# Kernel tuning notes

Measured on AMD Instinct MI355X. Metric: run time of the kernel, lower is better.

The kernel has to match this reference:

```python
import jax, jax.numpy as jnp
import numpy as np

THRESHOLD = 0.1
N_HEAD = 16
NEG_INF = -1e9


def setup_inputs() -> dict:
    key = jax.random.key(0)
    ks = jax.random.split(key, 8)
    B, T, C = 2, 2048, 1024
    H, D, R = N_HEAD, C // N_HEAD, 8
    return {
        "x": jax.random.normal(ks[0], (B, T, C), dtype=jnp.float32),
        "W_attn": jax.random.normal(ks[1], (C, 3 * C), dtype=jnp.float32) * 0.02,
        "W_proj": jax.random.normal(ks[2], (C, C), dtype=jnp.float32) * 0.02,
        "W_recip": jax.random.normal(ks[3], (D, R), dtype=jnp.float32) * 0.02,
        "w_std": jax.random.uniform(ks[4], (H,), dtype=jnp.float32),
        "w_rec": jax.random.uniform(ks[5], (H,), dtype=jnp.float32),
        "w_disc": jax.random.uniform(ks[6], (H,), dtype=jnp.float32),
        "d_bias": jax.random.normal(ks[7], (H, T), dtype=jnp.float32) * 0.02,
    }


def reference(x, W_attn, W_proj, W_recip, w_std, w_rec, w_disc, d_bias):
    B, T, C = x.shape
    H = N_HEAD
    D = C // H
    R = W_recip.shape[1]
    D_std = D - R

    # QKV projection (Linear without bias)
    qkv = x @ W_attn  # [B,T,3C]
    q, k, v = jnp.split(qkv, 3, axis=2)

    def to_heads(t):
        return t.reshape(B, T, H, D).transpose(0, 2, 1, 3)  # [B,H,T,D]

    q, k, v = to_heads(q), to_heads(k), to_heads(v)

    # low-rank reciprocal projections
    QW = q @ W_recip  # [B,H,T,R]
    KW = k @ W_recip

    ws = jnp.sqrt(jnp.clip(w_std, 1e-8))[:, None, None]  # [H,1,1]
    wr = jnp.sqrt(jnp.clip(w_rec, 1e-8))[:, None, None]
    use_ra = (w_rec > THRESHOLD)[:, None, None]  # [H,1,1]

    # RA heads: augmented Q/K = [ws*Q_std | wr*KW] / [ws*K_std | wr*QW]
    q_aug = jnp.concatenate([ws * q[..., :D_std], wr * KW], axis=-1)
    k_aug = jnp.concatenate([ws * k[..., :D_std], wr * QW], axis=-1)
    q_eff = jnp.where(use_ra, q_aug, ws * q)
    k_eff = jnp.where(use_ra, k_aug, ws * k)

    # mean-centered discoverability column bias: [1,H,1,T]
    d = d_bias[:, :T]
    d = d - d.mean(axis=-1, keepdims=True)
    bias = (d * w_disc[:, None])[None, :, None, :]

    scale = 1.0 / jnp.sqrt(jnp.asarray(D, dtype=x.dtype))
    scores = jnp.einsum("bhid,bhjd->bhij", q_eff, k_eff) * scale + bias
    causal = jnp.tril(jnp.ones((T, T), dtype=bool))
    scores = jnp.where(causal[None, None], scores, NEG_INF)
    attn = jax.nn.softmax(scores, axis=-1)
    out = jnp.einsum("bhij,bhjd->bhid", attn, v)  # [B,H,T,D]

    out = out.transpose(0, 2, 1, 3).reshape(B, T, C)
    return out @ W_proj
```

## Files before the change

### kernel.cpp

```cpp
#include <hip/hip_runtime.h>
#include <hip/hip_bf16.h>

#define DEVI __device__ __forceinline__

typedef __attribute__((ext_vector_type(8))) short short8;
typedef __attribute__((ext_vector_type(4))) short short4v;
typedef __attribute__((ext_vector_type(4))) float floatx4;

static constexpr int B_ = 2, T_ = 2048, C_ = 1024, H_ = 16, D_ = 64;
static constexpr float LOG2E = 1.44269504088896f;

DEVI float bf2f(unsigned short u) {
    union { unsigned int i; float f; } v; v.i = ((unsigned int)u) << 16; return v.f;
}
DEVI unsigned short f2bf(float f) {
    union { float f; unsigned int i; } v; v.f = f;
    unsigned int x = v.i;
    return (unsigned short)((x + 0x7fffu + ((x >> 16) & 1u)) >> 16);
}
DEVI unsigned int pk2bf(float lo, float hi) {
#if __has_builtin(__builtin_amdgcn_cvt_pk_bf16_f32)
    typedef __attribute__((ext_vector_type(2))) __bf16 bf16x2;
    union { bf16x2 v; unsigned int u; } r;
    r.v = __builtin_amdgcn_cvt_pk_bf16_f32(lo, hi);
    return r.u;
#else
    return (unsigned int)f2bf(lo) | ((unsigned int)f2bf(hi) << 16);
#endif
}
DEVI float fast_exp2(float x) {
#if __has_builtin(__builtin_amdgcn_exp2f)
    return __builtin_amdgcn_exp2f(x);
#else
    return __expf(x * 0.6931471805599453f);
#endif
}

DEVI void async16(const unsigned short* g, unsigned short* l) {
    __builtin_amdgcn_global_load_lds((const __attribute__((address_space(1))) void*)g,
                                     (__attribute__((address_space(3))) void*)l, 16, 0, 0);
}

DEVI void tr_body(const float* in, unsigned short* out, int K, int N, int bx, int by,
                  int tid, float (*tile)[65], float scale, bool skiphi) {
    int k0 = by * 64, n0 = bx * 64;
#pragma unroll
    for (int r = 0; r < 4; r++) {
        int ci = tid + r * 256;
        int row = ci >> 4, c4 = (ci & 15) * 4;
        float4 v = *(const float4*)&in[(size_t)(k0 + row) * N + n0 + c4];
        tile[row][c4 + 0] = v.x; tile[row][c4 + 1] = v.y;
        tile[row][c4 + 2] = v.z; tile[row][c4 + 3] = v.w;
    }
    __syncthreads();
#pragma unroll
    for (int r = 0; r < 2; r++) {
        int ci = tid + r * 256;
        int row = ci >> 3, c8 = (ci & 7) * 8;
        if (skiphi && row >= 56) continue;
        union { unsigned short u[8]; short8 s; } o;
#pragma unroll
        for (int j = 0; j < 8; j++) o.u[j] = f2bf(tile[c8 + j][row] * scale);
        *(short8*)&out[(size_t)(n0 + row) * K + k0 + c8] = o.s;
    }
}

__global__ __launch_bounds__(256) void k_prep(const float* __restrict__ x,
                                              const float* __restrict__ W_attn,
                                              const float* __restrict__ W_proj,
                                              const float* __restrict__ d_bias,
                                              const float* __restrict__ w_disc,
                                              const float* __restrict__ W_recip,
                                              const float* __restrict__ w_std,
                                              const float* __restrict__ w_rec,
                                              unsigned short* __restrict__ x_bf,
                                              unsigned short* __restrict__ wa_t,
                                              unsigned short* __restrict__ wp_t,
                                              float* __restrict__ bias) {
    __shared__ float tile[64][65];
    __shared__ float red[256];
    int bid = blockIdx.x, tid = threadIdx.x;
    if (bid < 2048) {
        int i = bid * 256 + tid;
        const float4* p = (const float4*)x + (size_t)i * 2;
        float4 a = p[0], b = p[1];
        union { unsigned short u[8]; short8 s; } r;
        r.u[0] = f2bf(a.x); r.u[1] = f2bf(a.y); r.u[2] = f2bf(a.z); r.u[3] = f2bf(a.w);
        r.u[4] = f2bf(b.x); r.u[5] = f2bf(b.y); r.u[6] = f2bf(b.z); r.u[7] = f2bf(b.w);
        *(short8*)&x_bf[(size_t)i * 8] = r.s;
    } else if (bid < 2816) {
        int idx = bid - 2048;
        int bx = idx % 48, by = idx / 48;
        int sec = bx >> 4, h = bx & 15;
        float ws = sqrtf(fmaxf(w_std[h], 1e-8f));
        float sc = (sec == 0) ? ws * (0.125f * LOG2E) : (sec == 1 ? ws : 1.0f);
        tr_body(W_attn, wa_t, 1024, 3072, bx, by, tid, tile, sc, sec < 2);
    } else if (bid < 3072) {
        int idx = bid - 2816;
        tr_body(W_proj, wp_t, 1024, 1024, idx & 15, idx >> 4, tid, tile, 1.0f, false);
    } else if (bid < 3088) {
        int h = bid - 3072;
        float s = 0.f;
        for (int t = tid; t < T_; t += 256) s += d_bias[h * T_ + t];
        red[tid] = s;
        __syncthreads();
        for (int st = 128; st > 0; st >>= 1) {
            if (tid < st) red[tid] += red[tid + st];
            __syncthreads();
        }
        float mean = red[0] * (1.0f / T_);
        float wd = w_disc[h] * LOG2E;
        for (int t = tid; t < T_; t += 256) bias[h * T_ + t] = (d_bias[h * T_ + t] - mean) * wd;
    } else {
        int idx = bid - 3088;
        int h = idx & 15, side = idx >> 4;
        float* WrS = &tile[0][0];
        for (int i = tid; i < 512; i += 256) WrS[i] = W_recip[i];
        __syncthreads();
        float wrv = sqrtf(fmaxf(w_rec[h], 1e-8f));
        float wsv = sqrtf(fmaxf(w_std[h], 1e-8f));
        bool ra = w_rec[h] > 0.1f;
        float sc = (side == 0 ? 0.125f * LOG2E : 1.0f) * (ra ? wrv : wsv);
        int dst0 = side * 1024 + h * 64 + 56;
        for (int kk = tid; kk < 1024; kk += 256) {
            const float* srow = W_attn + (size_t)kk * 3072;
            float out[8];
            if (ra) {
                int sc0 = (1 - side) * 1024 + h * 64;
#pragma unroll
                for (int r = 0; r < 8; r++) out[r] = 0.f;
                for (int dd = 0; dd < 64; dd++) {
                    float v = srow[sc0 + dd];
#pragma unroll
                    for (int r = 0; r < 8; r++) out[r] += v * WrS[dd * 8 + r];
                }
            } else {
                int sc0 = side * 1024 + h * 64 + 56;
#pragma unroll
                for (int r = 0; r < 8; r++) out[r] = srow[sc0 + r];
            }
#pragma unroll
            for (int r = 0; r < 8; r++)
                wa_t[(size_t)(dst0 + r) * 1024 + kk] = f2bf(sc * out[r]);
        }
    }
}

__global__ __launch_bounds__(256) void k_gemm_qkv(const unsigned short* __restrict__ A,
                                                  const unsigned short* __restrict__ Bt,
                                                  unsigned short* __restrict__ qe,
                                                  unsigned short* __restrict__ ke,
                                                  unsigned short* __restrict__ vt,
                                                  int M, int N, int K) {
    union SM {
        unsigned short buf[4][128 * 32];
        unsigned short stg[4][4096];
    };
    __shared__ __align__(16) SM sm;
    int b1d = blockIdx.y * 24 + blockIdx.x;
    int xcd = b1d & 7, i6 = b1d >> 3;
    int bx = (xcd & 1) * 12 + i6 % 12;
    int by = (xcd >> 1) * 8 + i6 / 12;
    int m0 = by * 128, n0 = bx * 128;
    int tid = threadIdx.x, l = tid & 63, w = tid >> 6;
    int wm = (w >> 1) * 64, wn = (w & 1) * 64;
    int lm = l & 15, lq = l >> 4;
    floatx4 acc[4][4];
#pragma unroll
    for (int a = 0; a < 4; a++)
#pragma unroll
        for (int b = 0; b < 4; b++) acc[a][b] = {0.f, 0.f, 0.f, 0.f};

    for (int k0 = 0; k0 < K; k0 += 64) {
        __syncthreads();
#pragma unroll
        for (int r = 0; r < 2; r++) {
            int ci = tid + r * 256;
            int row = ci >> 2, off = (ci & 3) * 8;
            async16(&A[(size_t)(m0 + row) * K + k0 + off],       &sm.buf[0][row * 32 + off]);
            async16(&A[(size_t)(m0 + row) * K + k0 + 32 + off],  &sm.buf[1][row * 32 + off]);
            async16(&Bt[(size_t)(n0 + row) * K + k0 + off],      &sm.buf[2][row * 32 + off]);
            async16(&Bt[(size_t)(n0 + row) * K + k0 + 32 + off], &sm.buf[3][row * 32 + off]);
        }
        __syncthreads();
#pragma unroll
        for (int half = 0; half < 2; half++) {
            const unsigned short* Ah = sm.buf[half];
            const unsigned short* Bh = sm.buf[2 + half];
            short8 af[4], bf[4];
#pragma unroll
            for (int t = 0; t < 4; t++) af[t] = *(short8*)&Ah[(wm + t * 16 + lm) * 32 + lq * 8];
#pragma unroll
            for (int t = 0; t < 4; t++) bf[t] = *(short8*)&Bh[(wn + t * 16 + lm) * 32 + lq * 8];
#pragma unroll
            for (int tm = 0; tm < 4; tm++)
#pragma unroll
                for (int tn = 0; tn < 4; tn++)
                    acc[tm][tn] = __builtin_amdgcn_mfma_f32_16x16x32_bf16(af[tm], bf[tn], acc[tm][tn], 0, 0, 0);
        }
    }
    __syncthreads();
    int sec = bx >> 3;
    int b = by >> 4;
    int head = ((n0 & 1023) >> 6) + (wn >> 6);
    size_t bhbase = (size_t)(b * 16 + head) * 131072;
    int tloc0 = (m0 & 2047) + wm;
    unsigned short* dst = (sec == 0) ? qe : (sec == 1) ? ke : vt;
    unsigned short* S = sm.stg[w];
    if (sec < 2) {
#pragma unroll
        for (int tm = 0; tm < 4; tm++)
#pragma unroll
            for (int tn = 0; tn < 4; tn++) {
                int base = tm * 1024 + (tn >> 1) * 512 + ((tn & 1) * 2 + (lm >> 3)) * 128 +
                           (lm & 7) + lq * 32;
#pragma unroll
                for (int r = 0; r < 4; r++) S[base + r * 8] = f2bf(acc[tm][tn][r]);
            }
    } else {
#pragma unroll
        for (int tm = 0; tm < 4; tm++)
#pragma unroll
            for (int tn = 0; tn < 4; tn++) {
                int base = (tm >> 1) * 2048 + tn * 512 + ((tm & 1) * 2 + (lq >> 1)) * 128 +
                           lm * 8 + (lq & 1) * 4;
                union { unsigned short u[4]; short4v s4; } o;
#pragma unroll
                for (int r = 0; r < 4; r++) o.u[r] = f2bf(acc[tm][tn][r]);
                *(short4v*)&S[base] = o.s4;
            }
    }
    size_t gbase = bhbase + ((sec < 2) ? (size_t)(tloc0 >> 4) * 1024
                                       : (size_t)(tloc0 >> 5) * 2048);
#pragma unroll
    for (int i = 0; i < 8; i++) {
        short8 v = *(const short8*)&S[(size_t)(i * 64 + l) * 8];
        *(short8*)&dst[gbase + (size_t)(i * 64 + l) * 8] = v;
    }
}

__global__ __launch_bounds__(256) void k_gemm64(const unsigned short* __restrict__ A,
                                                const unsigned short* __restrict__ Bt,
                                                float* __restrict__ C, int M, int N, int K) {
    __shared__ __align__(16) unsigned short As[2][128 * 32];
    __shared__ __align__(16) unsigned short Bs[2][64 * 32];
    int b1d = blockIdx.y * 16 + blockIdx.x;
    int xcd = b1d & 7, i6 = b1d >> 3;
    int bx = (xcd & 1) * 8 + (i6 & 7);
    int by = (xcd >> 1) * 8 + (i6 >> 3);
    int m0 = by * 128, n0 = bx * 64;
    int tid = threadIdx.x, l = tid & 63, w = tid >> 6;
    int wm = w * 32;
    int lm = l & 15, lq = l >> 4;
    floatx4 acc[2][4];
#pragma unroll
    for (int a = 0; a < 2; a++)
#pragma unroll
        for (int b = 0; b < 4; b++) acc[a][b] = {0.f, 0.f, 0.f, 0.f};

    for (int k0 = 0; k0 < K; k0 += 64) {
        __syncthreads();
#pragma unroll
        for (int r = 0; r < 2; r++) {
            int ci = tid + r * 256;
            int row = ci >> 2, off = (ci & 3) * 8;
            async16(&A[(size_t)(m0 + row) * K + k0 + off],      &As[0][row * 32 + off]);
            async16(&A[(size_t)(m0 + row) * K + k0 + 32 + off], &As[1][row * 32 + off]);
        }
        {
            int row = tid >> 2, off = (tid & 3) * 8;
            async16(&Bt[(size_t)(n0 + row) * K + k0 + off],      &Bs[0][row * 32 + off]);
            async16(&Bt[(size_t)(n0 + row) * K + k0 + 32 + off], &Bs[1][row * 32 + off]);
        }
        __syncthreads();
#pragma unroll
        for (int half = 0; half < 2; half++) {
            short8 af[2], bf[4];
#pragma unroll
            for (int t = 0; t < 2; t++) af[t] = *(short8*)&As[half][(wm + t * 16 + lm) * 32 + lq * 8];
#pragma unroll
            for (int t = 0; t < 4; t++) bf[t] = *(short8*)&Bs[half][(t * 16 + lm) * 32 + lq * 8];
#pragma unroll
            for (int tm = 0; tm < 2; tm++)
#pragma unroll
                for (int tn = 0; tn < 4; tn++)
                    acc[tm][tn] = __builtin_amdgcn_mfma_f32_16x16x32_bf16(af[tm], bf[tn], acc[tm][tn], 0, 0, 0);
        }
    }
#pragma unroll
    for (int tm = 0; tm < 2; tm++)
#pragma unroll
        for (int tn = 0; tn < 4; tn++) {
            int row = m0 + wm + tm * 16 + lq * 4;
            int col = n0 + tn * 16 + lm;
#pragma unroll
            for (int r = 0; r < 4; r++) C[(size_t)(row + r) * N + col] = acc[tm][tn][r];
        }
}

DEVI void exp_pack(float sv[4][4], float& l_part, unsigned int pk[4][2]) {
#pragma unroll
    for (int js = 0; js < 4; js++)
#pragma unroll
        for (int r = 0; r < 4; r++) {
            float p = fast_exp2(sv[js][r]);
            sv[js][r] = p;
            l_part += p;
        }
#pragma unroll
    for (int js = 0; js < 4; js++) {
        pk[js][0] = pk2bf(sv[js][0], sv[js][1]);
        pk[js][1] = pk2bf(sv[js][2], sv[js][3]);
    }
}

DEVI short8 make_pf(const unsigned int pk[4][2], int c, int srcLo, int srcHi, bool hi) {
    int a0 = __shfl((int)pk[2 * c][0], srcLo);
    int a1 = __shfl((int)pk[2 * c][1], srcLo);
    int a2 = __shfl((int)pk[2 * c][0], srcHi);
    int a3 = __shfl((int)pk[2 * c][1], srcHi);
    int b0 = __shfl((int)pk[2 * c + 1][0], srcLo);
    int b1 = __shfl((int)pk[2 * c + 1][1], srcLo);
    int b2 = __shfl((int)pk[2 * c + 1][0], srcHi);
    int b3 = __shfl((int)pk[2 * c + 1][1], srcHi);
    union { int i[4]; short8 s; } pf;
    pf.i[0] = hi ? b0 : a0;
    pf.i[1] = hi ? b1 : a1;
    pf.i[2] = hi ? b2 : a2;
    pf.i[3] = hi ? b3 : a3;
    return pf.s;
}

struct KF { short8 lo[4]; short8 hi[4]; };

__global__ __launch_bounds__(256) void k_attn(const unsigned short* __restrict__ qe,
                                              const unsigned short* __restrict__ ke,
                                              const unsigned short* __restrict__ vt,
                                              const float* __restrict__ bias,
                                              unsigned short* __restrict__ obf) {
    __shared__ __align__(16) float psum[2][64][36];
    int b1d = blockIdx.y * 32 + blockIdx.x;
    int xcd = b1d & 7, j = b1d >> 3;
    int bh = xcd * 4 + (j >> 5);
    int pxq = j & 31;
    int b = bh >> 4, h = bh & 15;
    int tid = threadIdx.x, l = tid & 63, w = tid >> 6;
    int pairL = w >> 1;
    int phase = w & 1;
    int lm = l & 15, lq = l >> 4;
    int l8 = l * 8;
    const size_t hb = (size_t)bh * 131072;
    const unsigned short* qeh = qe + hb;
    const unsigned short* keh = ke + hb;
    const unsigned short* vth = vt + hb;
    const float* biash = bias + h * T_;

    int gA = pxq * 2 + pairL;
    int gB = 127 - gA;
    int itA = (gA >> 2) + 1, itB = (gB >> 2) + 1;
    int irowA = gA * 16 + lm, irowB = gB * 16 + lm;

    short8 qA0 = *(const short8*)(qeh + (size_t)gA * 1024 + l8);
    short8 qA1 = *(const short8*)(qeh + (size_t)gA * 1024 + 512 + l8);
    short8 qB0 = *(const short8*)(qeh + (size_t)gB * 1024 + l8);
    short8 qB1 = *(const short8*)(qeh + (size_t)gB * 1024 + 512 + l8);

    floatx4 OA[4], OB[4];
#pragma unroll
    for (int i = 0; i < 4; i++) { OA[i] = {0.f, 0.f, 0.f, 0.f}; OB[i] = {0.f, 0.f, 0.f, 0.f}; }
    float lA = 0.f, lB = 0.f;

    const int srcLo = ((lq & 1) * 2) * 16 + lm;
    const int srcHi = srcLo + 16;
    const bool hi = (lq >> 1) & 1;

    KF kfa, kfb;
#pragma unroll
    for (int js = 0; js < 4; js++) {
        const unsigned short* kp = keh + (size_t)phase * 4096 + (size_t)js * 1024 + l8;
        kfa.lo[js] = *(const short8*)kp;
        kfa.hi[js] = *(const short8*)(kp + 512);
    }

    auto step = [&](int s, KF& cur, KF& nxt) {
        int j0 = s * 64;
        bool doA = (s < itA);
        bool maskA = (s == itA - 1);
        bool maskB = (s == itB - 1);
        {
            const unsigned short* kb = keh + (size_t)(s + 2) * 4096 + l8;
#pragma unroll
            for (int js = 0; js < 4; js++) {
                nxt.lo[js] = *(const short8*)(kb + js * 1024);
                nxt.hi[js] = *(const short8*)(kb + js * 1024 + 512);
            }
        }
        short8 vfr[2][4];
#pragma unroll
        for (int c = 0; c < 2; c++)
#pragma unroll
            for (int dt = 0; dt < 4; dt++)
                vfr[c][dt] = *(const short8*)(vth + (size_t)((j0 >> 5) + c) * 2048 + dt * 512 + l8);
        float bv[4][4];
#pragma unroll
        for (int js = 0; js < 4; js++) {
            float4 bj = *(const float4*)&biash[j0 + js * 16 + lq * 4];
            bv[js][0] = bj.x; bv[js][1] = bj.y; bv[js][2] = bj.z; bv[js][3] = bj.w;
        }
        floatx4 sb4[4], sa4[4];
#pragma unroll
        for (int js = 0; js < 4; js++) {
            floatx4 sb = {0.f, 0.f, 0.f, 0.f};
            sb = __builtin_amdgcn_mfma_f32_16x16x32_bf16(cur.lo[js], qB0, sb, 0, 0, 0);
            sb = __builtin_amdgcn_mfma_f32_16x16x32_bf16(cur.hi[js], qB1, sb, 0, 0, 0);
            sb4[js] = sb;
        }
        if (doA) {
#pragma unroll
            for (int js = 0; js < 4; js++) {
                floatx4 sa = {0.f, 0.f, 0.f, 0.f};
                sa = __builtin_amdgcn_mfma_f32_16x16x32_bf16(cur.lo[js], qA0, sa, 0, 0, 0);
                sa = __builtin_amdgcn_mfma_f32_16x16x32_bf16(cur.hi[js], qA1, sa, 0, 0, 0);
                sa4[js] = sa;
            }
        }
        float svB[4][4];
#pragma unroll
        for (int js = 0; js < 4; js++)
#pragma unroll
            for (int r = 0; r < 4; r++) svB[js][r] = sb4[js][r] + bv[js][r];
        if (maskB) {
#pragma unroll
            for (int js = 0; js < 4; js++) {
                int jb = j0 + js * 16 + lq * 4;
#pragma unroll
                for (int r = 0; r < 4; r++)
                    if (jb + r > irowB) svB[js][r] = -1e9f;
            }
        }
        unsigned int pkB[4][2];
        exp_pack(svB, lB, pkB);

        if (doA) {
            float svA[4][4];
#pragma unroll
            for (int js = 0; js < 4; js++)
#pragma unroll
                for (int r = 0; r < 4; r++) svA[js][r] = sa4[js][r] + bv[js][r];
            if (maskA) {
#pragma unroll
                for (int js = 0; js < 4; js++) {
                    int jb = j0 + js * 16 + lq * 4;
#pragma unroll
                    for (int r = 0; r < 4; r++)
                        if (jb + r > irowA) svA[js][r] = -1e9f;
                }
            }
            unsigned int pkA[4][2];
            exp_pack(svA, lA, pkA);
#pragma unroll
            for (int c = 0; c < 2; c++) {
                short8 pfA = make_pf(pkA, c, srcLo, srcHi, hi);
                short8 pfB = make_pf(pkB, c, srcLo, srcHi, hi);
#pragma unroll
                for (int dt = 0; dt < 4; dt++) {
                    OA[dt] = __builtin_amdgcn_mfma_f32_16x16x32_bf16(vfr[c][dt], pfA, OA[dt], 0, 0, 0);
                    OB[dt] = __builtin_amdgcn_mfma_f32_16x16x32_bf16(vfr[c][dt], pfB, OB[dt], 0, 0, 0);
                }
            }
        } else {
#pragma unroll
            for (int c = 0; c < 2; c++) {
                short8 pfB = make_pf(pkB, c, srcLo, srcHi, hi);
#pragma unroll
                for (int dt = 0; dt < 4; dt++)
                    OB[dt] = __builtin_amdgcn_mfma_f32_16x16x32_bf16(vfr[c][dt], pfB, OB[dt], 0, 0, 0);
            }
        }
    };

    int s = phase;
    for (; s + 2 < itB; s += 4) {
        step(s, kfa, kfb);
        step(s + 2, kfb, kfa);
    }
    if (s < itB) step(s, kfa, kfb);

    if (phase == 1) {
        float* dst = psum[pairL][l];
#pragma unroll
        for (int dt = 0; dt < 4; dt++) *(floatx4*)&dst[dt * 4] = OA[dt];
#pragma unroll
        for (int dt = 0; dt < 4; dt++) *(floatx4*)&dst[16 + dt * 4] = OB[dt];
        dst[32] = lA; dst[33] = lB;
    }
    __syncthreads();
    if (phase == 1) return;
    {
        const float* src = psum[pairL][l];
#pragma unroll
        for (int dt = 0; dt < 4; dt++) {
            OA[dt] += *(const floatx4*)&src[dt * 4];
            OB[dt] += *(const floatx4*)&src[16 + dt * 4];
        }
        lA += src[32]; lB += src[33];
    }

    lA += __shfl_xor(lA, 16); lA += __shfl_xor(lA, 32);
    lB += __shfl_xor(lB, 16); lB += __shfl_xor(lB, 32);
    {
        float inv = 1.0f / lA;
        unsigned short* orow = obf + (size_t)(b * T_ + irowA) * C_ + h * 64;
#pragma unroll
        for (int dt = 0; dt < 4; dt++) {
            union { unsigned short u[4]; short4v s4; } o;
#pragma unroll
            for (int r = 0; r < 4; r++) o.u[r] = f2bf(OA[dt][r] * inv);
            *(short4v*)&orow[dt * 16 + lq * 4] = o.s4;
        }
    }
    {
        float inv = 1.0f / lB;
        unsigned short* orow = obf + (size_t)(b * T_ + irowB) * C_ + h * 64;
#pragma unroll
        for (int dt = 0; dt < 4; dt++) {
            union { unsigned short u[4]; short4v s4; } o;
#pragma unroll
            for (int r = 0; r < 4; r++) o.u[r] = f2bf(OB[dt][r] * inv);
            *(short4v*)&orow[dt * 16 + lq * 4] = o.s4;
        }
    }
}

extern "C" void kernel_launch(void* const* d_in, const int* in_sizes, int n_in,
                              void* d_out, int out_size, void* d_ws, size_t ws_size,
                              hipStream_t stream) {
    const float* x       = (const float*)d_in[0];
    const float* W_attn  = (const float*)d_in[1];
    const float* W_proj  = (const float*)d_in[2];
    const float* W_recip = (const float*)d_in[3];
    const float* w_std   = (const float*)d_in[4];
    const float* w_rec   = (const float*)d_in[5];
    const float* w_disc  = (const float*)d_in[6];
    const float* d_bias  = (const float*)d_in[7];

    char* ws = (char*)d_ws;
    size_t o = 0;
    unsigned short* x_bf = (unsigned short*)(ws + o); o += (size_t)4096 * 1024 * 2;
    unsigned short* wa_t = (unsigned short*)(ws + o); o += (size_t)3072 * 1024 * 2;
    unsigned short* wp_t = (unsigned short*)(ws + o); o += (size_t)1024 * 1024 * 2;
    unsigned short* qe   = (unsigned short*)(ws + o); o += (size_t)32 * 2048 * 64 * 2;
    unsigned short* ke   = (unsigned short*)(ws + o); o += (size_t)32 * 2048 * 64 * 2;
    unsigned short* vt   = (unsigned short*)(ws + o); o += (size_t)32 * 2048 * 64 * 2;
    unsigned short* obf  = (unsigned short*)(ws + o); o += (size_t)4096 * 1024 * 2;
    float* bias          = (float*)(ws + o);          o += (size_t)16 * 2048 * 4;

    k_prep<<<3120, 256, 0, stream>>>(x, W_attn, W_proj, d_bias, w_disc, W_recip, w_std, w_rec,
                                     x_bf, wa_t, wp_t, bias);
    k_gemm_qkv<<<dim3(24, 32), 256, 0, stream>>>(x_bf, wa_t, qe, ke, vt, 4096, 3072, 1024);
    k_attn<<<dim3(32, 32), 256, 0, stream>>>(qe, ke, vt, bias, obf);
    k_gemm64<<<dim3(16, 32), 256, 0, stream>>>(obf, wp_t, (float*)d_out, 4096, 1024, 1024);
}
```

Before: 192.6 us.

## Move W_proj transpose and bias prep into QKV GEMM launch; deepen k_gemm64 K-step

The W_proj transpose and the discoverability-bias blocks move out of the prep kernel and become extra blocks appended to the QKV GEMM grid. This shortens the prep kernel and lets that work run alongside the GEMM's tail, since it is only needed by the later attention and projection kernels. Separately, the output projection GEMM now loads 128 K-columns per synchronisation instead of 64, halving the barrier count at the cost of doubled LDS use per block. The extra blocks share the GEMM's shared-memory union, and the larger LDS footprint could reduce occupancy.

```diff
diff --git a/kernel.cpp b/kernel.cpp
--- a/kernel.cpp
+++ b/kernel.cpp
@@ -65,20 +65,29 @@
     }
 }
 
+DEVI void bias_body(const float* d_bias, const float* w_disc, float* bias,
+                    int h, int tid, float* red) {
+    float s = 0.f;
+    for (int t = tid; t < T_; t += 256) s += d_bias[h * T_ + t];
+    red[tid] = s;
+    __syncthreads();
+    for (int st = 128; st > 0; st >>= 1) {
+        if (tid < st) red[tid] += red[tid + st];
+        __syncthreads();
+    }
+    float mean = red[0] * (1.0f / T_);
+    float wd = w_disc[h] * LOG2E;
+    for (int t = tid; t < T_; t += 256) bias[h * T_ + t] = (d_bias[h * T_ + t] - mean) * wd;
+}
+
 __global__ __launch_bounds__(256) void k_prep(const float* __restrict__ x,
                                               const float* __restrict__ W_attn,
-                                              const float* __restrict__ W_proj,
-                                              const float* __restrict__ d_bias,
-                                              const float* __restrict__ w_disc,
                                               const float* __restrict__ W_recip,
                                               const float* __restrict__ w_std,
                                               const float* __restrict__ w_rec,
                                               unsigned short* __restrict__ x_bf,
-                                              unsigned short* __restrict__ wa_t,
-                                              unsigned short* __restrict__ wp_t,
-                                              float* __restrict__ bias) {
+                                              unsigned short* __restrict__ wa_t) {
     __shared__ float tile[64][65];
-    __shared__ float red[256];
     int bid = blockIdx.x, tid = threadIdx.x;
     if (bid < 2048) {
         int i = bid * 256 + tid;
@@ -95,24 +104,8 @@
         float ws = sqrtf(fmaxf(w_std[h], 1e-8f));
         float sc = (sec == 0) ? ws * (0.125f * LOG2E) : (sec == 1 ? ws : 1.0f);
         tr_body(W_attn, wa_t, 1024, 3072, bx, by, tid, tile, sc, sec < 2);
-    } else if (bid < 3072) {
+    } else {
         int idx = bid - 2816;
-        tr_body(W_proj, wp_t, 1024, 1024, idx & 15, idx >> 4, tid, tile, 1.0f, false);
-    } else if (bid < 3088) {
-        int h = bid - 3072;
-        float s = 0.f;
-        for (int t = tid; t < T_; t += 256) s += d_bias[h * T_ + t];
-        red[tid] = s;
-        __syncthreads();
-        for (int st = 128; st > 0; st >>= 1) {
-            if (tid < st) red[tid] += red[tid + st];
-            __syncthreads();
-        }
-        float mean = red[0] * (1.0f / T_);
-        float wd = w_disc[h] * LOG2E;
-        for (int t = tid; t < T_; t += 256) bias[h * T_ + t] = (d_bias[h * T_ + t] - mean) * wd;
-    } else {
-        int idx = bid - 3088;
         int h = idx & 15, side = idx >> 4;
         float* WrS = &tile[0][0];
         for (int i = tid; i < 512; i += 256) WrS[i] = W_recip[i];
@@ -148,21 +141,37 @@
 
 __global__ __launch_bounds__(256) void k_gemm_qkv(const unsigned short* __restrict__ A,
                                                   const unsigned short* __restrict__ Bt,
+                                                  const float* __restrict__ W_proj,
+                                                  const float* __restrict__ d_bias,
+                                                  const float* __restrict__ w_disc,
                                                   unsigned short* __restrict__ qe,
                                                   unsigned short* __restrict__ ke,
                                                   unsigned short* __restrict__ vt,
+                                                  unsigned short* __restrict__ wp_t,
+                                                  float* __restrict__ bias,
                                                   int M, int N, int K) {
     union SM {
         unsigned short buf[4][128 * 32];
         unsigned short stg[4][4096];
+        struct { float tile[64][65]; float red[256]; } p;
     };
     __shared__ __align__(16) SM sm;
-    int b1d = blockIdx.y * 24 + blockIdx.x;
+    int bid = blockIdx.x, tid = threadIdx.x;
+    if (bid >= 768) {
+        if (bid < 1024) {
+            int idx = bid - 768;
+            tr_body(W_proj, wp_t, 1024, 1024, idx & 15, idx >> 4, tid, sm.p.tile, 1.0f, false);
+        } else {
+            bias_body(d_bias, w_disc, bias, bid - 1024, tid, sm.p.red);
+        }
+        return;
+    }
+    int b1d = bid;
     int xcd = b1d & 7, i6 = b1d >> 3;
     int bx = (xcd & 1) * 12 + i6 % 12;
     int by = (xcd >> 1) * 8 + i6 / 12;
     int m0 = by * 128, n0 = bx * 128;
-    int tid = threadIdx.x, l = tid & 63, w = tid >> 6;
+    int l = tid & 63, w = tid >> 6;
     int wm = (w >> 1) * 64, wn = (w & 1) * 64;
     int lm = l & 15, lq = l >> 4;
     floatx4 acc[4][4];
@@ -242,8 +251,8 @@
 __global__ __launch_bounds__(256) void k_gemm64(const unsigned short* __restrict__ A,
                                                 const unsigned short* __restrict__ Bt,
                                                 float* __restrict__ C, int M, int N, int K) {
-    __shared__ __align__(16) unsigned short As[2][128 * 32];
-    __shared__ __align__(16) unsigned short Bs[2][64 * 32];
+    __shared__ __align__(16) unsigned short As[4][128 * 32];
+    __shared__ __align__(16) unsigned short Bs[4][64 * 32];
     int b1d = blockIdx.y * 16 + blockIdx.x;
     int xcd = b1d & 7, i6 = b1d >> 3;
     int bx = (xcd & 1) * 8 + (i6 & 7);
@@ -258,28 +267,30 @@
 #pragma unroll
         for (int b = 0; b < 4; b++) acc[a][b] = {0.f, 0.f, 0.f, 0.f};
 
-    for (int k0 = 0; k0 < K; k0 += 64) {
+    for (int k0 = 0; k0 < K; k0 += 128) {
         __syncthreads();
 #pragma unroll
         for (int r = 0; r < 2; r++) {
             int ci = tid + r * 256;
             int row = ci >> 2, off = (ci & 3) * 8;
-            async16(&A[(size_t)(m0 + row) * K + k0 + off],      &As[0][row * 32 + off]);
-            async16(&A[(size_t)(m0 + row) * K + k0 + 32 + off], &As[1][row * 32 + off]);
+#pragma unroll
+            for (int q = 0; q < 4; q++)
+                async16(&A[(size_t)(m0 + row) * K + k0 + q * 32 + off], &As[q][row * 32 + off]);
         }
         {
             int row = tid >> 2, off = (tid & 3) * 8;
-            async16(&Bt[(size_t)(n0 + row) * K + k0 + off],      &Bs[0][row * 32 + off]);
-            async16(&Bt[(size_t)(n0 + row) * K + k0 + 32 + off], &Bs[1][row * 32 + off]);
+#pragma unroll
+            for (int q = 0; q < 4; q++)
+                async16(&Bt[(size_t)(n0 + row) * K + k0 + q * 32 + off], &Bs[q][row * 32 + off]);
         }
         __syncthreads();
 #pragma unroll
-        for (int half = 0; half < 2; half++) {
+        for (int q = 0; q < 4; q++) {
             short8 af[2], bf[4];
 #pragma unroll
-            for (int t = 0; t < 2; t++) af[t] = *(short8*)&As[half][(wm + t * 16 + lm) * 32 + lq * 8];
-#pragma unroll
-            for (int t = 0; t < 4; t++) bf[t] = *(short8*)&Bs[half][(t * 16 + lm) * 32 + lq * 8];
+            for (int t = 0; t < 2; t++) af[t] = *(short8*)&As[q][(wm + t * 16 + lm) * 32 + lq * 8];
+#pragma unroll
+            for (int t = 0; t < 4; t++) bf[t] = *(short8*)&Bs[q][(t * 16 + lm) * 32 + lq * 8];
 #pragma unroll
             for (int tm = 0; tm < 2; tm++)
 #pragma unroll
@@ -555,9 +566,9 @@
     unsigned short* obf  = (unsigned short*)(ws + o); o += (size_t)4096 * 1024 * 2;
     float* bias          = (float*)(ws + o);          o += (size_t)16 * 2048 * 4;
 
-    k_prep<<<3120, 256, 0, stream>>>(x, W_attn, W_proj, d_bias, w_disc, W_recip, w_std, w_rec,
-                                     x_bf, wa_t, wp_t, bias);
-    k_gemm_qkv<<<dim3(24, 32), 256, 0, stream>>>(x_bf, wa_t, qe, ke, vt, 4096, 3072, 1024);
+    k_prep<<<2848, 256, 0, stream>>>(x, W_attn, W_recip, w_std, w_rec, x_bf, wa_t);
+    k_gemm_qkv<<<1040, 256, 0, stream>>>(x_bf, wa_t, W_proj, d_bias, w_disc,
+                                         qe, ke, vt, wp_t, bias, 4096, 3072, 1024);
     k_attn<<<dim3(32, 32), 256, 0, stream>>>(qe, ke, vt, bias, obf);
     k_gemm64<<<dim3(16, 32), 256, 0, stream>>>(obf, wp_t, (float*)d_out, 4096, 1024, 1024);
 }
```

After: 191.7 us (median of 2 runs). About the same (-0.4%).
